# Optimization experiments

Hardware: AMD Instinct MI355X
Metric: run time of the kernel (lower is better)

## Reference

```python
import jax, jax.numpy as jnp
import numpy as np
import math

IN_DIM = 3
WIDTH = 256
DEPTH = 6
OUT_DIM = 1
W0_FIRST = 30.0
W0_HIDDEN = 1.0
N_POINTS = 1048576


def _uniform(key, shape, bound):
    return jax.random.uniform(key, shape, dtype=jnp.float32, minval=-bound, maxval=bound)


def setup_inputs() -> dict:
    key = jax.random.key(0)
    ks = jax.random.split(key, 8)
    xyt = jax.random.uniform(ks[0], (N_POINTS, IN_DIM), dtype=jnp.float32, minval=-1.0, maxval=1.0)
    # first layer: bound = 1/in_features
    W0 = _uniform(ks[1], (WIDTH, IN_DIM), 1.0 / IN_DIM)
    b0 = jnp.zeros((WIDTH,), jnp.float32)
    # hidden layers: bound = sqrt(6/width)/w0_hidden
    hb = math.sqrt(6.0 / WIDTH) / W0_HIDDEN
    W1 = _uniform(ks[2], (WIDTH, WIDTH), hb)
    b1 = jnp.zeros((WIDTH,), jnp.float32)
    W2 = _uniform(ks[3], (WIDTH, WIDTH), hb)
    b2 = jnp.zeros((WIDTH,), jnp.float32)
    W3 = _uniform(ks[4], (WIDTH, WIDTH), hb)
    b3 = jnp.zeros((WIDTH,), jnp.float32)
    W4 = _uniform(ks[5], (WIDTH, WIDTH), hb)
    b4 = jnp.zeros((WIDTH,), jnp.float32)
    Wf = _uniform(ks[6], (OUT_DIM, WIDTH), hb)
    bf = jnp.zeros((OUT_DIM,), jnp.float32)
    return {"xyt": xyt, "W0": W0, "b0": b0, "W1": W1, "b1": b1,
            "W2": W2, "b2": b2, "W3": W3, "b3": b3, "W4": W4, "b4": b4,
            "Wf": Wf, "bf": bf}


def reference(xyt, W0, b0, W1, b1, W2, b2, W3, b3, W4, b4, Wf, bf):
    # SineLayer: sin(w0 * (x @ W^T + b)); torch Linear weight is [out, in]
    h = jnp.sin(W0_FIRST * (xyt @ W0.T + b0))          # [N, 256]
    for W, b in ((W1, b1), (W2, b2), (W3, b3), (W4, b4)):
        h = jnp.sin(W0_HIDDEN * (h @ W.T + b))          # [N, 256]
    out = h @ Wf.T + bf                                  # [N, 1]
    return out.squeeze(-1)                               # [N]
```

## Files before the change

### kernel.cpp

```cpp
#include <hip/hip_runtime.h>

typedef _Float16 half8 __attribute__((ext_vector_type(8)));
typedef _Float16 half4 __attribute__((ext_vector_type(4)));
typedef __fp16  fp16x2 __attribute__((ext_vector_type(2)));
typedef float f32x4 __attribute__((ext_vector_type(4)));
typedef float f32x16 __attribute__((ext_vector_type(16)));

#define NPB 128
#define THREADS 512
#define INV2PI 0.15915494309189535f
#define W0SCALE (30.0f * INV2PI)
#define SMEM_BYTES (65536 + 384*4 + 256*4)


__device__ __forceinline__ half4 pk4(float a, float b, float c, float d) {
    fp16x2 lo = __builtin_amdgcn_cvt_pkrtz(a, b);
    fp16x2 hi = __builtin_amdgcn_cvt_pkrtz(c, d);
    half4 r;
    r[0] = (_Float16)lo[0]; r[1] = (_Float16)lo[1];
    r[2] = (_Float16)hi[0]; r[3] = (_Float16)hi[1];
    return r;
}

__global__ void convert_weights(const float* __restrict__ W1, const float* __restrict__ W2,
                                const float* __restrict__ W3, const float* __restrict__ W4,
                                _Float16* __restrict__ Wc) {
    int tid = blockIdx.x * 256 + threadIdx.x;
    int l   = tid >> 16;
    int rem = tid & 65535;
    int n = rem >> 8, k = rem & 255;
    const float* W = (l == 0) ? W1 : (l == 1) ? W2 : (l == 2) ? W3 : W4;
    int kc = k >> 5, kl = k & 31;
    Wc[l * 65536 + kc * 8192 + n * 32 + kl] = (_Float16)(W[rem] * INV2PI);
}

__launch_bounds__(THREADS, 4)
__global__ void siren_fused(const float* __restrict__ xyt,
                            const float* __restrict__ W0,
                            const float* __restrict__ b0,
                            const _Float16* __restrict__ Wc,
                            const float* __restrict__ b1,
                            const float* __restrict__ b2,
                            const float* __restrict__ b3,
                            const float* __restrict__ b4,
                            const float* __restrict__ Wf,
                            const float* __restrict__ bfin,
                            float* __restrict__ out)
{
    extern __shared__ _Float16 smem[];
    _Float16* hbuf = smem;
    float* xs   = (float*)(smem + 32768);
    float* wf_s = xs + 384;

    const int tid  = threadIdx.x;
    const int lane = tid & 63;
    const int wv   = tid >> 6;
    const int fq   = wv & 3;
    const int ph   = wv >> 2;
    const int l31  = lane & 31;
    const int o4   = lane >> 5;
    const int l7   = lane & 7;
    const int gm0  = blockIdx.x * NPB;

    if (tid < 384) xs[tid] = xyt[gm0 * 3 + tid];
    if (tid < 256) wf_s[tid] = Wf[tid];
    __syncthreads();

    {
        const int fg = lane;
        const int p0 = wv * 16;
        float w[4][3], bb[4];
        #pragma unroll
        for (int c = 0; c < 4; ++c) {
            const int n = fg * 4 + c;
            w[c][0] = W0[n * 3 + 0] * W0SCALE;
            w[c][1] = W0[n * 3 + 1] * W0SCALE;
            w[c][2] = W0[n * 3 + 2] * W0SCALE;
            bb[c]   = b0[n] * W0SCALE;
        }
        #pragma unroll 4
        for (int p = 0; p < 16; ++p) {
            const int pt = p0 + p;
            const float x0 = xs[pt * 3], x1 = xs[pt * 3 + 1], x2 = xs[pt * 3 + 2];
            float z0 = fmaf(w[0][0], x0, fmaf(w[0][1], x1, fmaf(w[0][2], x2, bb[0])));
            float z1 = fmaf(w[1][0], x0, fmaf(w[1][1], x1, fmaf(w[1][2], x2, bb[1])));
            float z2 = fmaf(w[2][0], x0, fmaf(w[2][1], x1, fmaf(w[2][2], x2, bb[2])));
            float z3 = fmaf(w[3][0], x0, fmaf(w[3][1], x1, fmaf(w[3][2], x2, bb[3])));
            half4 hv = pk4(__builtin_amdgcn_sinf(z0), __builtin_amdgcn_sinf(z1),
                           __builtin_amdgcn_sinf(z2), __builtin_amdgcn_sinf(z3));
            *(half4*)&hbuf[pt * 256 + (((fg >> 1) ^ (pt & 7)) << 3) + (fg & 1) * 4] = hv;
        }
    }

    const int m8  = (l7 & ~1) | (o4 ^ (l7 & 1));
    const int vb0 = (ph * 64 + l31) * 256;
    const int vb1 = vb0 + 32 * 256;
    const int ar0 = (fq * 64 + l31) * 32 + o4 * 8;
    const int ar1 = ar0 + 32 * 32;

    half8 ring[2][2];
    {
        const _Float16* wl = Wc;
        #pragma unroll
        for (int s = 0; s < 2; ++s) {
            ring[s][0] = *(const half8*)&wl[(s >> 1) * 8192 + (s & 1) * 16 + ar0];
            ring[s][1] = *(const half8*)&wl[(s >> 1) * 8192 + (s & 1) * 16 + ar1];
        }
    }

    #pragma unroll
    for (int l = 0; l < 4; ++l) {
        const float* bl = (l == 0) ? b1 : (l == 1) ? b2 : (l == 2) ? b3 : b4;
        const _Float16* wl = Wc + l * 65536;

        f32x16 acc[2][2];
        #pragma unroll
        for (int i = 0; i < 2; ++i) {
            #pragma unroll
            for (int q = 0; q < 4; ++q) {
                f32x4 bb = *(const f32x4*)&bl[fq * 64 + i * 32 + q * 8 + o4 * 4];
                bb *= INV2PI;
                #pragma unroll
                for (int r = 0; r < 4; ++r) {
                    acc[i][0][q * 4 + r] = bb[r];
                    acc[i][1][q * 4 + r] = bb[r];
                }
            }
        }

        __syncthreads();

        #pragma unroll
        for (int ks = 0; ks < 16; ++ks) {
            const int boff = ((2 * ks) ^ m8) << 3;
            half8 b0f = *(const half8*)&hbuf[vb0 + boff];
            half8 b1f = *(const half8*)&hbuf[vb1 + boff];
            acc[0][0] = __builtin_amdgcn_mfma_f32_32x32x16_f16(ring[ks & 1][0], b0f, acc[0][0], 0, 0, 0);
            acc[0][1] = __builtin_amdgcn_mfma_f32_32x32x16_f16(ring[ks & 1][0], b1f, acc[0][1], 0, 0, 0);
            acc[1][0] = __builtin_amdgcn_mfma_f32_32x32x16_f16(ring[ks & 1][1], b0f, acc[1][0], 0, 0, 0);
            acc[1][1] = __builtin_amdgcn_mfma_f32_32x32x16_f16(ring[ks & 1][1], b1f, acc[1][1], 0, 0, 0);
            if (ks < 14) {
                ring[ks & 1][0] = *(const half8*)&wl[((ks + 2) >> 1) * 8192 + ((ks + 2) & 1) * 16 + ar0];
                ring[ks & 1][1] = *(const half8*)&wl[((ks + 2) >> 1) * 8192 + ((ks + 2) & 1) * 16 + ar1];
            } else if (l < 3) {
                const _Float16* wn = wl + 65536;
                const int s = ks - 14;
                ring[s][0] = *(const half8*)&wn[(s & 1) * 16 + ar0];
                ring[s][1] = *(const half8*)&wn[(s & 1) * 16 + ar1];
            }
        }

        __syncthreads();

        #pragma unroll
        for (int i = 0; i < 2; ++i)
            #pragma unroll
            for (int j = 0; j < 2; ++j) {
                const int pt = ph * 64 + j * 32 + l31;
                #pragma unroll
                for (int q = 0; q < 4; ++q) {
                    half4 hv = pk4(__builtin_amdgcn_sinf(acc[i][j][q * 4 + 0]),
                                   __builtin_amdgcn_sinf(acc[i][j][q * 4 + 1]),
                                   __builtin_amdgcn_sinf(acc[i][j][q * 4 + 2]),
                                   __builtin_amdgcn_sinf(acc[i][j][q * 4 + 3]));
                    const int g = fq * 8 + i * 4 + q;
                    *(half4*)&hbuf[pt * 256 + ((g ^ l7) << 3) + o4 * 4] = hv;
                }
            }
    }

    __syncthreads();

    {
        const int m = tid >> 2, q = tid & 3;
        float sum = 0.f;
        #pragma unroll
        for (int i = 0; i < 8; ++i) {
            half8 hv = *(const half8*)&hbuf[m * 256 + (((q * 8 + i) ^ (m & 7)) << 3)];
            const int nb = q * 64 + i * 8;
            #pragma unroll
            for (int jj = 0; jj < 8; ++jj)
                sum = fmaf((float)hv[jj], wf_s[nb + jj], sum);
        }
        sum += __shfl_down(sum, 2);
        sum += __shfl_down(sum, 1);
        if (q == 0) out[gm0 + m] = sum + bfin[0];
    }
}

extern "C" void kernel_launch(void* const* d_in, const int* in_sizes, int n_in,
                              void* d_out, int out_size, void* d_ws, size_t ws_size,
                              hipStream_t stream) {
    const float* xyt = (const float*)d_in[0];
    const float* W0  = (const float*)d_in[1];
    const float* b0  = (const float*)d_in[2];
    const float* W1  = (const float*)d_in[3];
    const float* b1  = (const float*)d_in[4];
    const float* W2  = (const float*)d_in[5];
    const float* b2  = (const float*)d_in[6];
    const float* W3  = (const float*)d_in[7];
    const float* b3  = (const float*)d_in[8];
    const float* W4  = (const float*)d_in[9];
    const float* b4  = (const float*)d_in[10];
    const float* Wf  = (const float*)d_in[11];
    const float* bf  = (const float*)d_in[12];
    float* out = (float*)d_out;
    _Float16* Wc = (_Float16*)d_ws;

    (void)hipFuncSetAttribute((const void*)siren_fused,
                        hipFuncAttributeMaxDynamicSharedMemorySize, SMEM_BYTES);

    convert_weights<<<1024, 256, 0, stream>>>(W1, W2, W3, W4, Wc);

    const int N = in_sizes[0] / 3;
    siren_fused<<<N / NPB, THREADS, SMEM_BYTES, stream>>>(
        xyt, W0, b0, Wc, b1, b2, b3, b4, Wf, bf, out);
}
```

Baseline: 733.7 us.

## Halve block to 64 points with static LDS and prefetch LDS fragments

After: 695.6 us. 5.2% less time.

```diff
diff --git a/kernel.cpp b/kernel.cpp
--- a/kernel.cpp
+++ b/kernel.cpp
@@ -6,11 +6,10 @@
 typedef float f32x4 __attribute__((ext_vector_type(4)));
 typedef float f32x16 __attribute__((ext_vector_type(16)));
 
-#define NPB 128
-#define THREADS 512
+#define NPB 64
+#define THREADS 256
 #define INV2PI 0.15915494309189535f
 #define W0SCALE (30.0f * INV2PI)
-#define SMEM_BYTES (65536 + 384*4 + 256*4)
 
 
 __device__ __forceinline__ half4 pk4(float a, float b, float c, float d) {
@@ -47,24 +46,34 @@
                             const float* __restrict__ bfin,
                             float* __restrict__ out)
 {
-    extern __shared__ _Float16 smem[];
-    _Float16* hbuf = smem;
-    float* xs   = (float*)(smem + 32768);
-    float* wf_s = xs + 384;
+    __shared__ _Float16 hbuf[NPB * 256];
+    __shared__ float    xs[NPB * 3];
+    __shared__ float    wf_s[256];
 
     const int tid  = threadIdx.x;
     const int lane = tid & 63;
     const int wv   = tid >> 6;
-    const int fq   = wv & 3;
-    const int ph   = wv >> 2;
     const int l31  = lane & 31;
     const int o4   = lane >> 5;
     const int l7   = lane & 7;
     const int gm0  = blockIdx.x * NPB;
 
-    if (tid < 384) xs[tid] = xyt[gm0 * 3 + tid];
-    if (tid < 256) wf_s[tid] = Wf[tid];
+    if (tid < NPB * 3) xs[tid] = xyt[gm0 * 3 + tid];
+    wf_s[tid] = Wf[tid];
     __syncthreads();
+
+    const int m8  = (l7 & ~1) | (o4 ^ (l7 & 1));
+    const int vb0 = l31 * 256;
+    const int vb1 = vb0 + 32 * 256;
+    const int ar0 = (wv * 64 + l31) * 32 + o4 * 8;
+    const int ar1 = ar0 + 32 * 32;
+
+    half8 ring[2][2];
+    #pragma unroll
+    for (int s = 0; s < 2; ++s) {
+        ring[s][0] = *(const half8*)&Wc[s * 16 + ar0];
+        ring[s][1] = *(const half8*)&Wc[s * 16 + ar1];
+    }
 
     {
         const int fg = lane;
@@ -92,22 +101,6 @@
         }
     }
 
-    const int m8  = (l7 & ~1) | (o4 ^ (l7 & 1));
-    const int vb0 = (ph * 64 + l31) * 256;
-    const int vb1 = vb0 + 32 * 256;
-    const int ar0 = (fq * 64 + l31) * 32 + o4 * 8;
-    const int ar1 = ar0 + 32 * 32;
-
-    half8 ring[2][2];
-    {
-        const _Float16* wl = Wc;
-        #pragma unroll
-        for (int s = 0; s < 2; ++s) {
-            ring[s][0] = *(const half8*)&wl[(s >> 1) * 8192 + (s & 1) * 16 + ar0];
-            ring[s][1] = *(const half8*)&wl[(s >> 1) * 8192 + (s & 1) * 16 + ar1];
-        }
-    }
-
     #pragma unroll
     for (int l = 0; l < 4; ++l) {
         const float* bl = (l == 0) ? b1 : (l == 1) ? b2 : (l == 2) ? b3 : b4;
@@ -118,7 +111,7 @@
         for (int i = 0; i < 2; ++i) {
             #pragma unroll
             for (int q = 0; q < 4; ++q) {
-                f32x4 bb = *(const f32x4*)&bl[fq * 64 + i * 32 + q * 8 + o4 * 4];
+                f32x4 bb = *(const f32x4*)&bl[wv * 64 + i * 32 + q * 8 + o4 * 4];
                 bb *= INV2PI;
                 #pragma unroll
                 for (int r = 0; r < 4; ++r) {
@@ -130,24 +123,31 @@
 
         __syncthreads();
 
+        half8 b0c = *(const half8*)&hbuf[vb0 + ((0 ^ m8) << 3)];
+        half8 b1c = *(const half8*)&hbuf[vb1 + ((0 ^ m8) << 3)];
+
         #pragma unroll
         for (int ks = 0; ks < 16; ++ks) {
-            const int boff = ((2 * ks) ^ m8) << 3;
-            half8 b0f = *(const half8*)&hbuf[vb0 + boff];
-            half8 b1f = *(const half8*)&hbuf[vb1 + boff];
-            acc[0][0] = __builtin_amdgcn_mfma_f32_32x32x16_f16(ring[ks & 1][0], b0f, acc[0][0], 0, 0, 0);
-            acc[0][1] = __builtin_amdgcn_mfma_f32_32x32x16_f16(ring[ks & 1][0], b1f, acc[0][1], 0, 0, 0);
-            acc[1][0] = __builtin_amdgcn_mfma_f32_32x32x16_f16(ring[ks & 1][1], b0f, acc[1][0], 0, 0, 0);
-            acc[1][1] = __builtin_amdgcn_mfma_f32_32x32x16_f16(ring[ks & 1][1], b1f, acc[1][1], 0, 0, 0);
+            half8 b0n, b1n;
+            if (ks < 15) {
+                const int boff = ((2 * (ks + 1)) ^ m8) << 3;
+                b0n = *(const half8*)&hbuf[vb0 + boff];
+                b1n = *(const half8*)&hbuf[vb1 + boff];
+            }
+            acc[0][0] = __builtin_amdgcn_mfma_f32_32x32x16_f16(ring[ks & 1][0], b0c, acc[0][0], 0, 0, 0);
+            acc[0][1] = __builtin_amdgcn_mfma_f32_32x32x16_f16(ring[ks & 1][0], b1c, acc[0][1], 0, 0, 0);
+            acc[1][0] = __builtin_amdgcn_mfma_f32_32x32x16_f16(ring[ks & 1][1], b0c, acc[1][0], 0, 0, 0);
+            acc[1][1] = __builtin_amdgcn_mfma_f32_32x32x16_f16(ring[ks & 1][1], b1c, acc[1][1], 0, 0, 0);
             if (ks < 14) {
                 ring[ks & 1][0] = *(const half8*)&wl[((ks + 2) >> 1) * 8192 + ((ks + 2) & 1) * 16 + ar0];
                 ring[ks & 1][1] = *(const half8*)&wl[((ks + 2) >> 1) * 8192 + ((ks + 2) & 1) * 16 + ar1];
             } else if (l < 3) {
                 const _Float16* wn = wl + 65536;
                 const int s = ks - 14;
-                ring[s][0] = *(const half8*)&wn[(s & 1) * 16 + ar0];
-                ring[s][1] = *(const half8*)&wn[(s & 1) * 16 + ar1];
-            }
+                ring[s][0] = *(const half8*)&wn[s * 16 + ar0];
+                ring[s][1] = *(const half8*)&wn[s * 16 + ar1];
+            }
+            b0c = b0n; b1c = b1n;
         }
 
         __syncthreads();
@@ -156,14 +156,14 @@
         for (int i = 0; i < 2; ++i)
             #pragma unroll
             for (int j = 0; j < 2; ++j) {
-                const int pt = ph * 64 + j * 32 + l31;
+                const int pt = j * 32 + l31;
                 #pragma unroll
                 for (int q = 0; q < 4; ++q) {
                     half4 hv = pk4(__builtin_amdgcn_sinf(acc[i][j][q * 4 + 0]),
                                    __builtin_amdgcn_sinf(acc[i][j][q * 4 + 1]),
                                    __builtin_amdgcn_sinf(acc[i][j][q * 4 + 2]),
                                    __builtin_amdgcn_sinf(acc[i][j][q * 4 + 3]));
-                    const int g = fq * 8 + i * 4 + q;
+                    const int g = wv * 8 + i * 4 + q;
                     *(half4*)&hbuf[pt * 256 + ((g ^ l7) << 3) + o4 * 4] = hv;
                 }
             }
@@ -207,12 +207,9 @@
     float* out = (float*)d_out;
     _Float16* Wc = (_Float16*)d_ws;
 
-    (void)hipFuncSetAttribute((const void*)siren_fused,
-                        hipFuncAttributeMaxDynamicSharedMemorySize, SMEM_BYTES);
-
     convert_weights<<<1024, 256, 0, stream>>>(W1, W2, W3, W4, Wc);
 
     const int N = in_sizes[0] / 3;
-    siren_fused<<<N / NPB, THREADS, SMEM_BYTES, stream>>>(
+    siren_fused<<<N / NPB, THREADS, 0, stream>>>(
         xyt, W0, b0, Wc, b1, b2, b3, b4, Wf, bf, out);
 }
```
